# Kernel tuning notes

Measured on AMD Instinct MI355X. Metric: run time of the kernel, lower is better.

The kernel has to match this reference:

```python
import jax, jax.numpy as jnp
import numpy as np
import math

N, E = 10000, 640000
IN, HID, OUT, EF = 64, 64, 64, 16


def setup_inputs() -> dict:
    key = jax.random.key(0)
    ks = jax.random.split(key, 16)
    def lin(k, fan_in, fan_out):
        return jax.random.normal(k, (fan_in, fan_out), jnp.float32) / np.sqrt(fan_in)
    return {
        "node_feat": jax.random.normal(ks[0], (N, IN), jnp.float32),
        "coord_feat": jax.random.normal(ks[1], (N, 3), jnp.float32),
        "edge_feat": jax.random.normal(ks[2], (E, EF), jnp.float32),
        "W_e1": lin(ks[3], 2 * IN + EF + 1, HID), "b_e1": jnp.zeros((HID,), jnp.float32),
        "W_e2": lin(ks[4], HID, HID), "b_e2": jnp.zeros((HID,), jnp.float32),
        "W_n1": lin(ks[5], IN + HID, HID), "b_n1": jnp.zeros((HID,), jnp.float32),
        "W_n2": lin(ks[6], HID, OUT), "b_n2": jnp.zeros((OUT,), jnp.float32),
        "W_q": lin(ks[7], IN, HID),
        "W_k": lin(ks[8], IN + EF + 1, HID),
        "src": jax.random.randint(ks[9], (E,), 0, N, jnp.int32),
        "dst": jax.random.randint(ks[10], (E,), 0, N, jnp.int32),
    }


def reference(node_feat, coord_feat, edge_feat,
              W_e1, b_e1, W_e2, b_e2, W_n1, b_n1, W_n2, b_n2,
              W_q, W_k, src, dst):
    silu = jax.nn.silu
    # per-edge gathers
    h_src = node_feat[src]                      # [E, IN]
    h_dst = node_feat[dst]                      # [E, IN]
    x_diff = coord_feat[src] - coord_feat[dst]  # [E, 3]
    dist = jnp.sqrt(jnp.sum(x_diff * x_diff, axis=1, keepdims=True))  # [E, 1]
    # edge MLP message
    f = jnp.concatenate([h_src, h_dst, dist, edge_feat], axis=-1)      # [E, 2*IN+1+EF]
    msg_h = silu(silu(f @ W_e1 + b_e1) @ W_e2 + b_e2)                  # [E, HID]
    # attention score (QK dot)
    k_raw = jnp.concatenate([h_src, dist, edge_feat], axis=-1)         # [E, IN+1+EF]
    msg_k = k_raw @ W_k                                                # [E, HID]
    msg_q = h_dst @ W_q                                                # [E, HID]
    e = jnp.sum(msg_k * msg_q, axis=-1) / math.sqrt(HID)               # [E]
    # segment softmax over incoming edges of each dst node
    e_max = jax.ops.segment_max(e, dst, num_segments=N)                # [N]
    e_exp = jnp.exp(e - e_max[dst])                                    # [E]
    denom = jax.ops.segment_sum(e_exp, dst, num_segments=N)            # [N]
    att = e_exp / denom[dst]                                           # [E]
    # attention-weighted scatter-sum aggregation
    h_neigh = jax.ops.segment_sum(msg_h * att[:, None], dst, num_segments=N)  # [N, HID]
    # node MLP
    h = silu(jnp.concatenate([node_feat, h_neigh], axis=-1) @ W_n1 + b_n1) @ W_n2 + b_n2
    return h
```

## Files before the change

### kernel.cpp

```cpp
#include <hip/hip_runtime.h>

#define NN 10000
#define NE 640000

typedef __attribute__((ext_vector_type(8))) short bf16x8;
typedef __attribute__((ext_vector_type(4))) short s16x4;
typedef __attribute__((ext_vector_type(4))) float f32x4;

#define MFMA __builtin_amdgcn_mfma_f32_16x16x32_bf16

static __device__ __forceinline__ float silu_f(float x) {
    return x / (1.f + __expf(-x));
}
static __device__ __forceinline__ short f2bf(float x) {
    union { float f; unsigned u; } v; v.f = x;
    unsigned r = (v.u + 0x7FFF + ((v.u >> 16) & 1)) >> 16;
    return (short)r;
}
static __device__ __forceinline__ float bf2f(short h) {
    union { float f; unsigned u; } v; v.u = ((unsigned)(unsigned short)h) << 16;
    return v.f;
}

__global__ __launch_bounds__(256) void k_hist(const int* __restrict__ dst,
                                              int* __restrict__ cnt) {
    int e = blockIdx.x * 256 + threadIdx.x;
    if (e < NE) atomicAdd(&cnt[dst[e]], 1);
}

__global__ __launch_bounds__(256) void k_scan(const int* __restrict__ cnt,
                                              int* __restrict__ row_start,
                                              int* __restrict__ cursor) {
    __shared__ int part[256];
    __shared__ int base[257];
    const int t = threadIdx.x;
    int loc[40];
    int s = 0;
    #pragma unroll
    for (int i = 0; i < 40; i++) {
        int idx = t * 40 + i;
        int v = (idx < NN) ? cnt[idx] : 0;
        loc[i] = s; s += v;
    }
    part[t] = s;
    __syncthreads();
    if (t == 0) {
        int a = 0;
        for (int j = 0; j < 256; j++) { base[j] = a; a += part[j]; }
        base[256] = a;
    }
    __syncthreads();
    #pragma unroll
    for (int i = 0; i < 40; i++) {
        int idx = t * 40 + i;
        if (idx < NN) { int v = base[t] + loc[i]; row_start[idx] = v; cursor[idx] = v; }
    }
    if (t == 0) row_start[NN] = base[256];
}

__global__ __launch_bounds__(256) void k_scatter(const int* __restrict__ dst,
                                                 int* __restrict__ cursor,
                                                 int* __restrict__ perm) {
    int e = blockIdx.x * 256 + threadIdx.x;
    if (e < NE) {
        int d = dst[e];
        int p = atomicAdd(&cursor[d], 1);
        perm[p] = e;
    }
}

__global__ __launch_bounds__(256) void k_pack(
    const int* __restrict__ perm, const int* __restrict__ src,
    const int* __restrict__ dst, const float* __restrict__ ef,
    const float* __restrict__ coord,
    int* __restrict__ src_s, unsigned short* __restrict__ dist_s,
    unsigned short* __restrict__ efs)
{
    int p = blockIdx.x * 256 + threadIdx.x;
    if (p >= NE) return;
    const int e = perm[p];
    const int s = src[e];
    const int d = dst[e];

    const float dx = coord[s*3+0] - coord[d*3+0];
    const float dy = coord[s*3+1] - coord[d*3+1];
    const float dz = coord[s*3+2] - coord[d*3+2];
    const float dist = sqrtf(dx*dx + dy*dy + dz*dz);

    src_s[p] = s;
    dist_s[p] = (unsigned short)f2bf(dist);

    const float4* ep = (const float4*)(ef + (size_t)e*16);
    #pragma unroll
    for (int j = 0; j < 4; j++) {
        float4 a = ep[j];
        s16x4 p4;
        p4[0] = f2bf(a.x); p4[1] = f2bf(a.y); p4[2] = f2bf(a.z); p4[3] = f2bf(a.w);
        *(s16x4*)&efs[(size_t)p*16 + j*4] = p4;
    }
}

__global__ __launch_bounds__(256) void node_pre_kernel(
    const float* __restrict__ node_feat,
    const float* __restrict__ W_e1,
    const float* __restrict__ W_k,
    const float* __restrict__ W_q,
    short* __restrict__ nfb, float* __restrict__ B,
    float* __restrict__ G, float* __restrict__ EQn, float* __restrict__ WQn)
{
    __shared__ float sW1b[64*64];
    __shared__ float sWq[64*64];
    __shared__ float sWk[64*65];
    __shared__ float sWke[16*65];
    __shared__ __align__(16) float sx[4][64];
    __shared__ __align__(16) float sq[4][64];

    for (int i = threadIdx.x; i < 64*64; i += 256) {
        sW1b[i] = W_e1[64*64 + i];
        sWq[i]  = W_q[i];
        int c = i >> 6, j = i & 63;
        sWk[c*65 + j] = W_k[i];
    }
    for (int i = threadIdx.x; i < 16*64; i += 256) {
        int k = i >> 6, j = i & 63;
        sWke[k*65 + j] = W_k[(65 + k)*64 + j];
    }
    __syncthreads();

    const int wid = threadIdx.x >> 6;
    const int lane = threadIdx.x & 63;
    for (int n = blockIdx.x * 4 + wid; n < NN; n += gridDim.x * 4) {
        float x = node_feat[n*64 + lane];
        nfb[n*64 + lane] = f2bf(x);
        sx[wid][lane] = x;
        float b = 0.f, q = 0.f;
        #pragma unroll
        for (int i = 0; i < 64; i += 4) {
            float4 x4 = *(const float4*)&sx[wid][i];
            b += x4.x*sW1b[(i+0)*64+lane] + x4.y*sW1b[(i+1)*64+lane]
               + x4.z*sW1b[(i+2)*64+lane] + x4.w*sW1b[(i+3)*64+lane];
            q += x4.x*sWq[(i+0)*64+lane] + x4.y*sWq[(i+1)*64+lane]
               + x4.z*sWq[(i+2)*64+lane] + x4.w*sWq[(i+3)*64+lane];
        }
        B[n*64 + lane] = b;
        sq[wid][lane] = q;

        float g = 0.f;
        #pragma unroll
        for (int j = 0; j < 64; j += 4) {
            float4 q4 = *(const float4*)&sq[wid][j];
            g += q4.x*sWk[lane*65 + j]   + q4.y*sWk[lane*65 + j+1]
               + q4.z*sWk[lane*65 + j+2] + q4.w*sWk[lane*65 + j+3];
        }
        G[n*64 + lane] = g;

        float p = W_k[64*64 + lane] * q;
        #pragma unroll
        for (int off = 32; off; off >>= 1) p += __shfl_xor(p, off);
        if (lane == 0) WQn[n] = p;

        int kk = lane & 15, pp = lane >> 4;
        float s = 0.f;
        #pragma unroll
        for (int jj = 0; jj < 16; jj++) {
            int j = pp*16 + jj;
            s += sWke[kk*65 + j] * sq[wid][j];
        }
        s += __shfl_xor(s, 16); s += __shfl_xor(s, 32);
        if (lane < 16) EQn[n*16 + kk] = s;
    }
}

__global__ __launch_bounds__(512, 2) void edge_kernel(
    const short* __restrict__ nfb, const int* __restrict__ src_s,
    const unsigned short* __restrict__ dist_s,
    const unsigned short* __restrict__ efs, const int* __restrict__ row_start,
    const float* __restrict__ W_e1, const float* __restrict__ b_e1,
    const float* __restrict__ W_e2, const float* __restrict__ b_e2,
    const float* __restrict__ B, const float* __restrict__ G,
    const float* __restrict__ EQn, const float* __restrict__ WQn,
    float* __restrict__ hout)
{
    __shared__ short sW1T[64*104];
    __shared__ short sW2T[64*72];
    __shared__ short sX[8][16*104];
    __shared__ short sH1[8][16*72];
    __shared__ __align__(16) float sG[8][64];
    __shared__ __align__(16) float sEQ[8][16];

    const int tid = threadIdx.x;
    const int wid = tid >> 6, l = tid & 63;
    const int cl = l & 15, rg = l >> 4;
    const int er = l >> 2, q = l & 3;

    for (int i = tid; i < 64*104; i += 512) sW1T[i] = 0;
    __syncthreads();
    for (int i = tid; i < 64*82; i += 512) {
        int k = i >> 6, c = i & 63;
        float v;
        if (k < 64)       v = W_e1[k*64 + c];
        else if (k < 80)  v = W_e1[(129 + k - 64)*64 + c];
        else if (k == 80) v = W_e1[128*64 + c];
        else              v = b_e1[c];
        sW1T[c*104 + k] = f2bf(v);
    }
    for (int i = tid; i < 64*64; i += 512) {
        int k = i >> 6, c = i & 63;
        sW2T[c*72 + k] = f2bf(W_e2[k*64 + c]);
    }
    if (l < 16) {
        #pragma unroll
        for (int c = 82; c < 96; c++) sX[wid][l*104 + c] = 0;
        sX[wid][l*104 + 81] = (short)0x3F80;
    }
    __syncthreads();

    const int n = blockIdx.x * 8 + wid;
    const int beg = row_start[n], end = row_start[n+1];

    const size_t nb = (size_t)n*64;
    const float Bb0 = B[nb+cl],     Bb1 = B[nb+16+cl];
    const float Bb2 = B[nb+32+cl],  Bb3 = B[nb+48+cl];
    const float b20 = b_e2[cl],     b21 = b_e2[16+cl];
    const float b22 = b_e2[32+cl],  b23 = b_e2[48+cl];
    sG[wid][l] = G[nb + l];
    if (l < 16) sEQ[wid][l] = EQn[(size_t)n*16 + l];
    const float wq = WQn[n];

    float hs0 = 0.f, hs1 = 0.f, hs2 = 0.f, hs3 = 0.f, den = 0.f;

    int idx = beg + er; if (idx > NE-1) idx = NE-1;
    int sN = src_s[idx];
    bf16x8 nfAN = *(const bf16x8*)&nfb[(size_t)sN*64 + q*8];
    bf16x8 nfBN = *(const bf16x8*)&nfb[(size_t)sN*64 + 32 + q*8];
    s16x4  efN  = *(const s16x4*)&efs[(size_t)idx*16 + q*4];
    unsigned short dN = dist_s[idx];

    for (int c0 = beg; c0 < end; c0 += 16) {
        bf16x8 nfA = nfAN, nfB = nfBN; s16x4 ef4 = efN;
        unsigned short dcur = dN;

        int idx2 = c0 + 16 + er; if (idx2 > NE-1) idx2 = NE-1;
        sN = src_s[idx2];
        nfAN = *(const bf16x8*)&nfb[(size_t)sN*64 + q*8];
        nfBN = *(const bf16x8*)&nfb[(size_t)sN*64 + 32 + q*8];
        efN  = *(const s16x4*)&efs[(size_t)idx2*16 + q*4];
        dN   = dist_s[idx2];

        const float dist = bf2f((short)dcur);
        float p_ = 0.f;
        #pragma unroll
        for (int i = 0; i < 8; i++) {
            p_ += bf2f(nfA[i]) * sG[wid][q*8 + i];
            p_ += bf2f(nfB[i]) * sG[wid][32 + q*8 + i];
        }
        #pragma unroll
        for (int i = 0; i < 4; i++)
            p_ += bf2f(ef4[i]) * sEQ[wid][q*4 + i];
        p_ += __shfl_xor(p_, 1); p_ += __shfl_xor(p_, 2);
        const float wgt = __expf((p_ + dist * wq) * 0.125f);

        *(bf16x8*)&sX[wid][er*104 + q*8]      = nfA;
        *(bf16x8*)&sX[wid][er*104 + 32 + q*8] = nfB;
        *(s16x4*)&sX[wid][er*104 + 64 + q*4]  = ef4;
        if (q == 0) sX[wid][er*104 + 80] = (short)dcur;

        bf16x8 ax0 = *(const bf16x8*)&sX[wid][cl*104 +  0 + rg*8];
        bf16x8 ax1 = *(const bf16x8*)&sX[wid][cl*104 + 32 + rg*8];
        bf16x8 ax2 = *(const bf16x8*)&sX[wid][cl*104 + 64 + rg*8];
        f32x4 a0 = {Bb0,Bb0,Bb0,Bb0}, a1 = {Bb1,Bb1,Bb1,Bb1};
        f32x4 a2 = {Bb2,Bb2,Bb2,Bb2}, a3 = {Bb3,Bb3,Bb3,Bb3};
        a0 = MFMA(ax0, *(const bf16x8*)&sW1T[( 0+cl)*104 +  0 + rg*8], a0, 0,0,0);
        a0 = MFMA(ax1, *(const bf16x8*)&sW1T[( 0+cl)*104 + 32 + rg*8], a0, 0,0,0);
        a0 = MFMA(ax2, *(const bf16x8*)&sW1T[( 0+cl)*104 + 64 + rg*8], a0, 0,0,0);
        a1 = MFMA(ax0, *(const bf16x8*)&sW1T[(16+cl)*104 +  0 + rg*8], a1, 0,0,0);
        a1 = MFMA(ax1, *(const bf16x8*)&sW1T[(16+cl)*104 + 32 + rg*8], a1, 0,0,0);
        a1 = MFMA(ax2, *(const bf16x8*)&sW1T[(16+cl)*104 + 64 + rg*8], a1, 0,0,0);
        a2 = MFMA(ax0, *(const bf16x8*)&sW1T[(32+cl)*104 +  0 + rg*8], a2, 0,0,0);
        a2 = MFMA(ax1, *(const bf16x8*)&sW1T[(32+cl)*104 + 32 + rg*8], a2, 0,0,0);
        a2 = MFMA(ax2, *(const bf16x8*)&sW1T[(32+cl)*104 + 64 + rg*8], a2, 0,0,0);
        a3 = MFMA(ax0, *(const bf16x8*)&sW1T[(48+cl)*104 +  0 + rg*8], a3, 0,0,0);
        a3 = MFMA(ax1, *(const bf16x8*)&sW1T[(48+cl)*104 + 32 + rg*8], a3, 0,0,0);
        a3 = MFMA(ax2, *(const bf16x8*)&sW1T[(48+cl)*104 + 64 + rg*8], a3, 0,0,0);
        #pragma unroll
        for (int r = 0; r < 4; r++) {
            int row = rg*4 + r;
            sH1[wid][row*72 +  0 + cl] = f2bf(silu_f(a0[r]));
            sH1[wid][row*72 + 16 + cl] = f2bf(silu_f(a1[r]));
            sH1[wid][row*72 + 32 + cl] = f2bf(silu_f(a2[r]));
            sH1[wid][row*72 + 48 + cl] = f2bf(silu_f(a3[r]));
        }

        bf16x8 ah0 = *(const bf16x8*)&sH1[wid][cl*72 + rg*8];
        bf16x8 ah1 = *(const bf16x8*)&sH1[wid][cl*72 + 32 + rg*8];
        f32x4 c0v = {b20,b20,b20,b20}, c1v = {b21,b21,b21,b21};
        f32x4 c2v = {b22,b22,b22,b22}, c3v = {b23,b23,b23,b23};
        c0v = MFMA(ah0, *(const bf16x8*)&sW2T[( 0+cl)*72 +      rg*8], c0v, 0,0,0);
        c0v = MFMA(ah1, *(const bf16x8*)&sW2T[( 0+cl)*72 + 32 + rg*8], c0v, 0,0,0);
        c1v = MFMA(ah0, *(const bf16x8*)&sW2T[(16+cl)*72 +      rg*8], c1v, 0,0,0);
        c1v = MFMA(ah1, *(const bf16x8*)&sW2T[(16+cl)*72 + 32 + rg*8], c1v, 0,0,0);
        c2v = MFMA(ah0, *(const bf16x8*)&sW2T[(32+cl)*72 +      rg*8], c2v, 0,0,0);
        c2v = MFMA(ah1, *(const bf16x8*)&sW2T[(32+cl)*72 + 32 + rg*8], c2v, 0,0,0);
        c3v = MFMA(ah0, *(const bf16x8*)&sW2T[(48+cl)*72 +      rg*8], c3v, 0,0,0);
        c3v = MFMA(ah1, *(const bf16x8*)&sW2T[(48+cl)*72 + 32 + rg*8], c3v, 0,0,0);

        #pragma unroll
        for (int r = 0; r < 4; r++) {
            int row = rg*4 + r;
            float wr = (c0 + row < end) ? __shfl(wgt, row << 2) : 0.f;
            hs0 += wr * silu_f(c0v[r]);
            hs1 += wr * silu_f(c1v[r]);
            hs2 += wr * silu_f(c2v[r]);
            hs3 += wr * silu_f(c3v[r]);
            den += wr;
        }
    }

    hs0 += __shfl_xor(hs0, 16); hs0 += __shfl_xor(hs0, 32);
    hs1 += __shfl_xor(hs1, 16); hs1 += __shfl_xor(hs1, 32);
    hs2 += __shfl_xor(hs2, 16); hs2 += __shfl_xor(hs2, 32);
    hs3 += __shfl_xor(hs3, 16); hs3 += __shfl_xor(hs3, 32);
    den += __shfl_xor(den, 16); den += __shfl_xor(den, 32);

    float v = (rg == 0) ? hs0 : (rg == 1) ? hs1 : (rg == 2) ? hs2 : hs3;
    hout[nb + l] = (den > 0.f) ? v / den : 0.f;
}

__global__ __launch_bounds__(256) void node_out_kernel(
    const float* __restrict__ node_feat,
    const float* __restrict__ W_n1, const float* __restrict__ b_n1,
    const float* __restrict__ W_n2, const float* __restrict__ b_n2,
    const float* __restrict__ hacc, float* __restrict__ out)
{
    __shared__ float sWn1[128*64];
    __shared__ float sWn2[64*64];
    __shared__ __align__(16) float sx[4][64], sg[4][64], st[4][64];

    for (int i = threadIdx.x; i < 128*64; i += 256) sWn1[i] = W_n1[i];
    for (int i = threadIdx.x; i < 64*64; i += 256)  sWn2[i] = W_n2[i];
    __syncthreads();

    const int wid = threadIdx.x >> 6;
    const int lane = threadIdx.x & 63;
    for (int n = blockIdx.x * 4 + wid; n < NN; n += gridDim.x * 4) {
        sx[wid][lane] = node_feat[n*64 + lane];
        sg[wid][lane] = hacc[n*64 + lane];

        float acc = b_n1[lane];
        #pragma unroll
        for (int i = 0; i < 64; i += 4) {
            float4 x4 = *(const float4*)&sx[wid][i];
            float4 g4 = *(const float4*)&sg[wid][i];
            acc += x4.x*sWn1[(i+0)*64+lane] + x4.y*sWn1[(i+1)*64+lane]
                 + x4.z*sWn1[(i+2)*64+lane] + x4.w*sWn1[(i+3)*64+lane];
            acc += g4.x*sWn1[(64+i+0)*64+lane] + g4.y*sWn1[(64+i+1)*64+lane]
                 + g4.z*sWn1[(64+i+2)*64+lane] + g4.w*sWn1[(64+i+3)*64+lane];
        }
        const float tt = silu_f(acc);
        st[wid][lane] = tt;

        float acc2 = b_n2[lane];
        #pragma unroll
        for (int i = 0; i < 64; i += 4) {
            float4 t4 = *(const float4*)&st[wid][i];
            acc2 += t4.x*sWn2[(i+0)*64+lane] + t4.y*sWn2[(i+1)*64+lane]
                  + t4.z*sWn2[(i+2)*64+lane] + t4.w*sWn2[(i+3)*64+lane];
        }
        out[n*64 + lane] = acc2;
    }
}

extern "C" void kernel_launch(void* const* d_in, const int* in_sizes, int n_in,
                              void* d_out, int out_size, void* d_ws, size_t ws_size,
                              hipStream_t stream) {
    const float* node_feat = (const float*)d_in[0];
    const float* coord     = (const float*)d_in[1];
    const float* edge_feat = (const float*)d_in[2];
    const float* W_e1 = (const float*)d_in[3];
    const float* b_e1 = (const float*)d_in[4];
    const float* W_e2 = (const float*)d_in[5];
    const float* b_e2 = (const float*)d_in[6];
    const float* W_n1 = (const float*)d_in[7];
    const float* b_n1 = (const float*)d_in[8];
    const float* W_n2 = (const float*)d_in[9];
    const float* b_n2 = (const float*)d_in[10];
    const float* W_q  = (const float*)d_in[11];
    const float* W_k  = (const float*)d_in[12];
    const int* src = (const int*)d_in[13];
    const int* dst = (const int*)d_in[14];
    float* out = (float*)d_out;

    float* ws = (float*)d_ws;
    short* nfb       = (short*)ws;
    float* B         = ws + 320000;
    float* G         = ws + 960000;
    float* EQn       = ws + 1600000;
    float* WQn       = ws + 1760000;
    int*   cnt       = (int*)(ws + 1770000);
    int*   row_start = (int*)(ws + 1780000);
    int*   cursor    = (int*)(ws + 1790004);
    int*   perm      = (int*)(ws + 1800004);
    int*   src_s     = (int*)(ws + 2440004);
    unsigned short* dist_s = (unsigned short*)(ws + 3080004);
    unsigned short* efs    = (unsigned short*)(ws + 3400004);
    float* hacc      = ws + 8520004;

    hipMemsetAsync(cnt, 0, NN * sizeof(int), stream);

    node_pre_kernel<<<625, 256, 0, stream>>>(node_feat, W_e1, W_k, W_q,
                                             nfb, B, G, EQn, WQn);
    k_hist<<<2500, 256, 0, stream>>>(dst, cnt);
    k_scan<<<1, 256, 0, stream>>>(cnt, row_start, cursor);
    k_scatter<<<2500, 256, 0, stream>>>(dst, cursor, perm);
    k_pack<<<2500, 256, 0, stream>>>(perm, src, dst, edge_feat, coord,
                                     src_s, dist_s, efs);
    edge_kernel<<<1250, 512, 0, stream>>>(nfb, src_s, dist_s, efs, row_start,
                                          W_e1, b_e1, W_e2, b_e2,
                                          B, G, EQn, WQn, hacc);
    node_out_kernel<<<625, 256, 0, stream>>>(node_feat, W_n1, b_n1, W_n2, b_n2,
                                             hacc, out);
}
```

Measured before the change: 367.3 us.

## Permute edge-MLP weight columns for packed bf16 stores and use fast SiLU

The W_e1 and W_e2 columns in LDS are permuted so each lane owns four contiguous output columns. This lets the hidden activations be packed with v_cvt_pk_bf16_f32 and written as one 8-byte LDS store, and the bias loads become single float4 reads. SiLU now uses a hardware reciprocal instead of a division. The scan kernel stages counts through LDS so its global reads and writes are coalesced. The node_pre and node_out grids are enlarged, which only stays correct if those kernels' indexing handles the larger grid; the reciprocal also slightly lowers precision.

```diff
diff --git a/kernel.cpp b/kernel.cpp
--- a/kernel.cpp
+++ b/kernel.cpp
@@ -11,6 +11,11 @@
 
 static __device__ __forceinline__ float silu_f(float x) {
     return x / (1.f + __expf(-x));
+}
+static __device__ __forceinline__ float silu_fast(float x) {
+    float d = 1.f + __expf(-x);
+    float r; asm("v_rcp_f32 %0, %1" : "=v"(r) : "v"(d));
+    return x * r;
 }
 static __device__ __forceinline__ short f2bf(float x) {
     union { float f; unsigned u; } v; v.f = x;
@@ -31,16 +36,19 @@
 __global__ __launch_bounds__(256) void k_scan(const int* __restrict__ cnt,
                                               int* __restrict__ row_start,
                                               int* __restrict__ cursor) {
+    __shared__ int sv[NN];
     __shared__ int part[256];
     __shared__ int base[257];
     const int t = threadIdx.x;
-    int loc[40];
+    for (int i = t; i < NN; i += 256) sv[i] = cnt[i];
+    __syncthreads();
     int s = 0;
     #pragma unroll
     for (int i = 0; i < 40; i++) {
         int idx = t * 40 + i;
-        int v = (idx < NN) ? cnt[idx] : 0;
-        loc[i] = s; s += v;
+        int v = (idx < NN) ? sv[idx] : 0;
+        if (idx < NN) sv[idx] = s;
+        s += v;
     }
     part[t] = s;
     __syncthreads();
@@ -50,10 +58,9 @@
         base[256] = a;
     }
     __syncthreads();
-    #pragma unroll
-    for (int i = 0; i < 40; i++) {
-        int idx = t * 40 + i;
-        if (idx < NN) { int v = base[t] + loc[i]; row_start[idx] = v; cursor[idx] = v; }
+    for (int i = t; i < NN; i += 256) {
+        int v = base[i / 40] + sv[i];
+        row_start[i] = v; cursor[i] = v;
     }
     if (t == 0) row_start[NN] = base[256];
 }
@@ -202,11 +209,13 @@
         else if (k < 80)  v = W_e1[(129 + k - 64)*64 + c];
         else if (k == 80) v = W_e1[128*64 + c];
         else              v = b_e1[c];
-        sW1T[c*104 + k] = f2bf(v);
+        int s = (c & 3) * 16 + (c >> 2);
+        sW1T[s*104 + k] = f2bf(v);
     }
     for (int i = tid; i < 64*64; i += 512) {
         int k = i >> 6, c = i & 63;
-        sW2T[c*72 + k] = f2bf(W_e2[k*64 + c]);
+        int s = (c & 3) * 16 + (c >> 2);
+        sW2T[s*72 + k] = f2bf(W_e2[k*64 + c]);
     }
     if (l < 16) {
         #pragma unroll
@@ -219,10 +228,8 @@
     const int beg = row_start[n], end = row_start[n+1];
 
     const size_t nb = (size_t)n*64;
-    const float Bb0 = B[nb+cl],     Bb1 = B[nb+16+cl];
-    const float Bb2 = B[nb+32+cl],  Bb3 = B[nb+48+cl];
-    const float b20 = b_e2[cl],     b21 = b_e2[16+cl];
-    const float b22 = b_e2[32+cl],  b23 = b_e2[48+cl];
+    const float4 Bb4 = *(const float4*)&B[nb + cl*4];
+    const float4 b24 = *(const float4*)&b_e2[cl*4];
     sG[wid][l] = G[nb + l];
     if (l < 16) sEQ[wid][l] = EQn[(size_t)n*16 + l];
     const float wq = WQn[n];
@@ -268,8 +275,8 @@
         bf16x8 ax0 = *(const bf16x8*)&sX[wid][cl*104 +  0 + rg*8];
         bf16x8 ax1 = *(const bf16x8*)&sX[wid][cl*104 + 32 + rg*8];
         bf16x8 ax2 = *(const bf16x8*)&sX[wid][cl*104 + 64 + rg*8];
-        f32x4 a0 = {Bb0,Bb0,Bb0,Bb0}, a1 = {Bb1,Bb1,Bb1,Bb1};
-        f32x4 a2 = {Bb2,Bb2,Bb2,Bb2}, a3 = {Bb3,Bb3,Bb3,Bb3};
+        f32x4 a0 = {Bb4.x,Bb4.x,Bb4.x,Bb4.x}, a1 = {Bb4.y,Bb4.y,Bb4.y,Bb4.y};
+        f32x4 a2 = {Bb4.z,Bb4.z,Bb4.z,Bb4.z}, a3 = {Bb4.w,Bb4.w,Bb4.w,Bb4.w};
         a0 = MFMA(ax0, *(const bf16x8*)&sW1T[( 0+cl)*104 +  0 + rg*8], a0, 0,0,0);
         a0 = MFMA(ax1, *(const bf16x8*)&sW1T[( 0+cl)*104 + 32 + rg*8], a0, 0,0,0);
         a0 = MFMA(ax2, *(const bf16x8*)&sW1T[( 0+cl)*104 + 64 + rg*8], a0, 0,0,0);
@@ -285,16 +292,19 @@
         #pragma unroll
         for (int r = 0; r < 4; r++) {
             int row = rg*4 + r;
-            sH1[wid][row*72 +  0 + cl] = f2bf(silu_f(a0[r]));
-            sH1[wid][row*72 + 16 + cl] = f2bf(silu_f(a1[r]));
-            sH1[wid][row*72 + 32 + cl] = f2bf(silu_f(a2[r]));
-            sH1[wid][row*72 + 48 + cl] = f2bf(silu_f(a3[r]));
+            float s0 = silu_fast(a0[r]), s1 = silu_fast(a1[r]);
+            float s2 = silu_fast(a2[r]), s3 = silu_fast(a3[r]);
+            unsigned lo, hi;
+            asm("v_cvt_pk_bf16_f32 %0, %1, %2" : "=v"(lo) : "v"(s0), "v"(s1));
+            asm("v_cvt_pk_bf16_f32 %0, %1, %2" : "=v"(hi) : "v"(s2), "v"(s3));
+            uint2 u; u.x = lo; u.y = hi;
+            *(uint2*)&sH1[wid][row*72 + cl*4] = u;
         }
 
         bf16x8 ah0 = *(const bf16x8*)&sH1[wid][cl*72 + rg*8];
         bf16x8 ah1 = *(const bf16x8*)&sH1[wid][cl*72 + 32 + rg*8];
-        f32x4 c0v = {b20,b20,b20,b20}, c1v = {b21,b21,b21,b21};
-        f32x4 c2v = {b22,b22,b22,b22}, c3v = {b23,b23,b23,b23};
+        f32x4 c0v = {b24.x,b24.x,b24.x,b24.x}, c1v = {b24.y,b24.y,b24.y,b24.y};
+        f32x4 c2v = {b24.z,b24.z,b24.z,b24.z}, c3v = {b24.w,b24.w,b24.w,b24.w};
         c0v = MFMA(ah0, *(const bf16x8*)&sW2T[( 0+cl)*72 +      rg*8], c0v, 0,0,0);
         c0v = MFMA(ah1, *(const bf16x8*)&sW2T[( 0+cl)*72 + 32 + rg*8], c0v, 0,0,0);
         c1v = MFMA(ah0, *(const bf16x8*)&sW2T[(16+cl)*72 +      rg*8], c1v, 0,0,0);
@@ -308,10 +318,10 @@
         for (int r = 0; r < 4; r++) {
             int row = rg*4 + r;
             float wr = (c0 + row < end) ? __shfl(wgt, row << 2) : 0.f;
-            hs0 += wr * silu_f(c0v[r]);
-            hs1 += wr * silu_f(c1v[r]);
-            hs2 += wr * silu_f(c2v[r]);
-            hs3 += wr * silu_f(c3v[r]);
+            hs0 += wr * silu_fast(c0v[r]);
+            hs1 += wr * silu_fast(c1v[r]);
+            hs2 += wr * silu_fast(c2v[r]);
+            hs3 += wr * silu_fast(c3v[r]);
             den += wr;
         }
     }
@@ -323,7 +333,7 @@
     den += __shfl_xor(den, 16); den += __shfl_xor(den, 32);
 
     float v = (rg == 0) ? hs0 : (rg == 1) ? hs1 : (rg == 2) ? hs2 : hs3;
-    hout[nb + l] = (den > 0.f) ? v / den : 0.f;
+    hout[nb + cl*4 + rg] = (den > 0.f) ? v / den : 0.f;
 }
 
 __global__ __launch_bounds__(256) void node_out_kernel(
@@ -407,8 +417,8 @@
 
     hipMemsetAsync(cnt, 0, NN * sizeof(int), stream);
 
-    node_pre_kernel<<<625, 256, 0, stream>>>(node_feat, W_e1, W_k, W_q,
-                                             nfb, B, G, EQn, WQn);
+    node_pre_kernel<<<2500, 256, 0, stream>>>(node_feat, W_e1, W_k, W_q,
+                                              nfb, B, G, EQn, WQn);
     k_hist<<<2500, 256, 0, stream>>>(dst, cnt);
     k_scan<<<1, 256, 0, stream>>>(cnt, row_start, cursor);
     k_scatter<<<2500, 256, 0, stream>>>(dst, cursor, perm);
@@ -417,6 +427,6 @@
     edge_kernel<<<1250, 512, 0, stream>>>(nfb, src_s, dist_s, efs, row_start,
                                           W_e1, b_e1, W_e2, b_e2,
                                           B, G, EQn, WQn, hacc);
-    node_out_kernel<<<625, 256, 0, stream>>>(node_feat, W_n1, b_n1, W_n2, b_n2,
-                                             hacc, out);
-}
+    node_out_kernel<<<2500, 256, 0, stream>>>(node_feat, W_n1, b_n1, W_n2, b_n2,
+                                              hacc, out);
+}
```

Measured after the change: 348.2 us. 5.2% less time.
